# Kernel tuning notes

Measured on AMD Instinct MI355X. Metric: run time of the kernel, lower is better.

The kernel has to match this reference:

```python
import jax, jax.numpy as jnp
import numpy as np

# static config matching init_kwargs / input_specs
SPATIAL = [(64, 64), (32, 32), (16, 16), (8, 8)]  # (H_l, W_l) per level
LEN = sum(h * w for h, w in SPATIAL)  # 5440
B, C, H, L, P = 4, 256, 8, 4, 4
DH = C // H
DFF = 1024
EPS = 1e-5


def layer_norm(x, g, b):
    m = x.mean(-1, keepdims=True)
    v = ((x - m) ** 2).mean(-1, keepdims=True)
    return (x - m) / jnp.sqrt(v + EPS) * g + b


def msda_core(value, sampling_locations, attn_weights):
    """Multi-scale deformable attention core (bilinear sample + weighted sum).
    value: [B, Len, H, DH]; sampling_locations: [B, Lq, H, L, P, 2] in [0,1];
    attn_weights: [B, Lq, H, L, P]. Returns [B, Lq, C].
    Matches grid_sample(bilinear, align_corners=False, padding_mode='zeros')."""
    Bn, Lq = sampling_locations.shape[0], sampling_locations.shape[1]
    out = jnp.zeros((Bn, H, Lq, DH), value.dtype)
    start = 0
    for l, (Hl, Wl) in enumerate(SPATIAL):
        vl = value[:, start:start + Hl * Wl]          # [B, Hl*Wl, H, DH]
        start += Hl * Wl
        vl = vl.transpose(0, 2, 1, 3)                  # [B, H, Hl*Wl, DH]
        loc = sampling_locations[:, :, :, l].transpose(0, 2, 1, 3, 4)  # [B,H,Lq,P,2]
        # align_corners=False: pixel = loc * size - 0.5
        px = loc[..., 0] * Wl - 0.5
        py = loc[..., 1] * Hl - 0.5
        x0 = jnp.floor(px); y0 = jnp.floor(py)
        wx1 = px - x0; wy1 = py - y0
        x0i = x0.astype(jnp.int32); y0i = y0.astype(jnp.int32)
        samp = jnp.zeros((Bn, H, Lq, P, DH), value.dtype)
        for dx, dy in ((0, 0), (1, 0), (0, 1), (1, 1)):
            ix = x0i + dx; iy = y0i + dy
            w = (wx1 if dx else 1.0 - wx1) * (wy1 if dy else 1.0 - wy1)
            valid = (ix >= 0) & (ix < Wl) & (iy >= 0) & (iy < Hl)
            idx = jnp.clip(iy, 0, Hl - 1) * Wl + jnp.clip(ix, 0, Wl - 1)  # [B,H,Lq,P]
            g = jnp.take_along_axis(vl, idx.reshape(Bn, H, -1)[..., None], axis=2)
            g = g.reshape(Bn, H, Lq, P, DH)
            samp = samp + g * (w * valid)[..., None]
        aw = attn_weights[:, :, :, l].transpose(0, 2, 1, 3)  # [B,H,Lq,P]
        out = out + (samp * aw[..., None]).sum(3)
    return out.transpose(0, 2, 1, 3).reshape(Bn, Lq, C)


def setup_inputs() -> dict:
    key = jax.random.key(0)
    ks = jax.random.split(key, 20)
    inp = {
        'src': jax.random.normal(ks[0], (B, LEN, C), jnp.float32),
        'pos': jax.random.normal(ks[1], (B, LEN, C), jnp.float32),
        'reference_points': jax.random.uniform(ks[2], (B, LEN, L, 2), jnp.float32),
        'spatial_shapes': jnp.array(SPATIAL, dtype=jnp.int32),
        'level_start_index': jnp.array(np.cumsum([0] + [h * w for h, w in SPATIAL[:-1]]), dtype=jnp.int32),
        'valid_ratios': jnp.ones((B, L, 2), jnp.float32),
        # MSDeformAttn params
        'w_off': jax.random.normal(ks[3], (C, H * L * P * 2), jnp.float32) * 0.01,
        'b_off': jax.random.normal(ks[4], (H * L * P * 2,), jnp.float32) * 0.5,
        'w_attn': jax.random.normal(ks[5], (C, H * L * P), jnp.float32) * 0.05,
        'b_attn': jnp.zeros((H * L * P,), jnp.float32),
        'w_val': jax.random.normal(ks[6], (C, C), jnp.float32) * 0.05,
        'b_val': jnp.zeros((C,), jnp.float32),
        'w_out': jax.random.normal(ks[7], (C, C), jnp.float32) * 0.05,
        'b_out': jnp.zeros((C,), jnp.float32),
        # norm1 + FFN + norm2 params
        'g1': jnp.ones((C,), jnp.float32), 'be1': jnp.zeros((C,), jnp.float32),
        'w1': jax.random.normal(ks[8], (C, DFF), jnp.float32) * 0.05,
        'b1': jnp.zeros((DFF,), jnp.float32),
        'w2': jax.random.normal(ks[9], (DFF, C), jnp.float32) * 0.05,
        'b2': jnp.zeros((C,), jnp.float32),
        'g2': jnp.ones((C,), jnp.float32), 'be2': jnp.zeros((C,), jnp.float32),
    }
    return inp


def reference(src, pos, reference_points, spatial_shapes, level_start_index, valid_ratios,
              w_off, b_off, w_attn, b_attn, w_val, b_val, w_out, b_out,
              g1, be1, w1, b1, w2, b2, g2, be2):
    Bn, Lq, _ = src.shape
    q = src + pos  # with_pos_embed
    off = (q @ w_off + b_off).reshape(Bn, Lq, H, L, P, 2)
    aw = jax.nn.softmax((q @ w_attn + b_attn).reshape(Bn, Lq, H, L * P), axis=-1)
    aw = aw.reshape(Bn, Lq, H, L, P)
    # offset normalizer is (W_l, H_l) per level
    norm = jnp.array([[w, h] for h, w in SPATIAL], dtype=src.dtype)  # [L, 2]
    loc = reference_points[:, :, None, :, None, :] + off / norm[None, None, None, :, None, :]
    value = (src @ w_val + b_val).reshape(Bn, Lq, H, DH)  # padding_mask is None
    attn_out = msda_core(value, loc, aw) @ w_out + b_out
    x = layer_norm(src + attn_out, g1, be1)
    ffn = jax.nn.relu(x @ w1 + b1) @ w2 + b2
    return layer_norm(x + ffn, g2, be2)
```

## Files before the change

### kernel.cpp

```cpp
#include <hip/hip_runtime.h>
#include <hip/hip_fp16.h>
#include <math.h>

#define LEN   5440
#define NTOK  21760
#define CDIM  256
#define HEADS 8
#define DFF   1024
#define LEPS  1e-5f

typedef __attribute__((ext_vector_type(8))) _Float16 f16x8;
typedef __attribute__((ext_vector_type(4))) float f32x4;

__device__ __forceinline__ float4 f4_add(float4 a, float4 b) {
    return make_float4(a.x + b.x, a.y + b.y, a.z + b.z, a.w + b.w);
}

__global__ __launch_bounds__(256) void pack_k(const float* __restrict__ w_off,
                                              const float* __restrict__ w_attn,
                                              const float* __restrict__ w_val,
                                              const float* __restrict__ b_off,
                                              const float* __restrict__ b_attn,
                                              const float* __restrict__ b_val,
                                              const float* __restrict__ w_out,
                                              const float* __restrict__ w1,
                                              const float* __restrict__ w2,
                                              __half* __restrict__ WcatT,
                                              __half* __restrict__ woutT,
                                              __half* __restrict__ w1T,
                                              __half* __restrict__ w2T,
                                              float* __restrict__ bcat) {
    const int i = blockIdx.x * 256 + threadIdx.x;
    if (i < 163840) {
        const int c = i >> 8, k = i & 255;
        float v;
        if (c < 256)      v = w_off[k * 256 + c];
        else if (c < 384) v = w_attn[k * 128 + (c - 256)];
        else              v = w_val[k * 256 + (c - 384)];
        WcatT[i] = __float2half(v);
    } else if (i < 229376) {
        const int j = i - 163840, c = j >> 8, k = j & 255;
        woutT[j] = __float2half(w_out[k * 256 + c]);
    } else if (i < 491520) {
        const int j = i - 229376, c = j >> 8, k = j & 255;
        w1T[j] = __float2half(w1[k * 1024 + c]);
    } else if (i < 753664) {
        const int j = i - 491520, c = j >> 10, k = j & 1023;
        w2T[j] = __float2half(w2[k * 256 + c]);
    }
    if (i < 640) {
        bcat[i] = (i < 256) ? b_off[i] : (i < 384) ? b_attn[i - 256] : b_val[i - 384];
    }
}

__global__ __launch_bounds__(256) void cvt_k(const float* __restrict__ src,
                                             const float* __restrict__ pos,
                                             __half* __restrict__ qh,
                                             __half* __restrict__ srch) {
    const size_t i = (size_t)blockIdx.x * 256 + threadIdx.x;
    float4 s = *(const float4*)&src[i * 4];
    float4 p = *(const float4*)&pos[i * 4];
    union { __half2 h[2]; uint2 u; } Q, S;
    Q.h[0] = __floats2half2_rn(s.x + p.x, s.y + p.y);
    Q.h[1] = __floats2half2_rn(s.z + p.z, s.w + p.w);
    S.h[0] = __floats2half2_rn(s.x, s.y);
    S.h[1] = __floats2half2_rn(s.z, s.w);
    *(uint2*)&qh[i * 4]   = Q.u;
    *(uint2*)&srch[i * 4] = S.u;
}

template <bool RELU, bool OUTF, bool OUTH>
__global__ __launch_bounds__(256) void hgemm_k(const __half* __restrict__ Aq,
                                               const __half* __restrict__ Av,
                                               const __half* __restrict__ Bt,
                                               const float* __restrict__ bias,
                                               float* __restrict__ Cf,
                                               __half* __restrict__ Ch,
                                               int Nn, int K, int colSwitch) {
    __shared__ __half As[128][40];
    __shared__ __half Bs[128][40];
    const int bx = blockIdx.x, by = blockIdx.y;
    const int tid = threadIdx.x;
    const int lane = tid & 63;
    const int wave = tid >> 6;
    const int wr = (wave >> 1) * 64;
    const int wc = (wave & 1) * 64;

    const __half* __restrict__ Ah = (bx * 128 < colSwitch) ? Aq : Av;
    const __half* Abase = Ah + (size_t)(by * 128) * K;
    const __half* Bbase = Bt + (size_t)(bx * 128) * K;

    const int srow = tid >> 1;
    const int sk = (tid & 1) * 16;

    f32x4 acc[4][4];
#pragma unroll
    for (int m = 0; m < 4; ++m)
#pragma unroll
        for (int n = 0; n < 4; ++n) acc[m][n] = (f32x4){0.f, 0.f, 0.f, 0.f};

    const int fr = lane & 15;
    const int fk = (lane >> 4) * 8;

    for (int k0 = 0; k0 < K; k0 += 32) {
        const uint4 a0 = *(const uint4*)&Abase[(size_t)srow * K + k0 + sk];
        const uint4 a1 = *(const uint4*)&Abase[(size_t)srow * K + k0 + sk + 8];
        const uint4 b0 = *(const uint4*)&Bbase[(size_t)srow * K + k0 + sk];
        const uint4 b1 = *(const uint4*)&Bbase[(size_t)srow * K + k0 + sk + 8];
        __syncthreads();
        *(uint4*)&As[srow][sk]     = a0;
        *(uint4*)&As[srow][sk + 8] = a1;
        *(uint4*)&Bs[srow][sk]     = b0;
        *(uint4*)&Bs[srow][sk + 8] = b1;
        __syncthreads();
        f16x8 af[4], bf[4];
#pragma unroll
        for (int m = 0; m < 4; ++m) af[m] = *(const f16x8*)&As[wr + m * 16 + fr][fk];
#pragma unroll
        for (int n = 0; n < 4; ++n) bf[n] = *(const f16x8*)&Bs[wc + n * 16 + fr][fk];
#pragma unroll
        for (int m = 0; m < 4; ++m)
#pragma unroll
            for (int n = 0; n < 4; ++n)
                acc[m][n] = __builtin_amdgcn_mfma_f32_16x16x32_f16(af[m], bf[n], acc[m][n], 0, 0, 0);
    }

    const int rowb = by * 128 + wr + (lane >> 4) * 4;
    const int colb = bx * 128 + wc + fr;
    float bn[4];
#pragma unroll
    for (int n = 0; n < 4; ++n) bn[n] = bias[colb + n * 16];
#pragma unroll
    for (int m = 0; m < 4; ++m) {
#pragma unroll
        for (int r = 0; r < 4; ++r) {
            const size_t ro = (size_t)(rowb + m * 16 + r) * Nn + colb;
#pragma unroll
            for (int n = 0; n < 4; ++n) {
                float v = acc[m][n][r] + bn[n];
                if (RELU) v = fmaxf(v, 0.f);
                if (OUTF) Cf[ro + n * 16] = v;
                if (OUTH) Ch[ro + n * 16] = __float2half(v);
            }
        }
    }
}

__global__ __launch_bounds__(256) void msda_kernel(const float* __restrict__ C1,
                                                   const float* __restrict__ refp,
                                                   __half* __restrict__ out) {
    const int tid  = threadIdx.x;
    const int g    = tid & 7;
    const int pair = tid >> 3;
    const int h    = pair & 7;
    const int n    = blockIdx.x * 4 + (pair >> 3);
    const int b    = n / LEN;
    const size_t rowb = (size_t)n * 640;

    float lg[16];
    float mx = -1e30f;
#pragma unroll
    for (int s = 0; s < 16; ++s) {
        lg[s] = C1[rowb + 256 + h * 16 + s];
        mx = fmaxf(mx, lg[s]);
    }
    float sum = 0.f;
#pragma unroll
    for (int s = 0; s < 16; ++s) {
        lg[s] = expf(lg[s] - mx);
        sum += lg[s];
    }
    const float inv = 1.f / sum;

    const int Wi[4] = {64, 32, 16, 8};
    const int st[4] = {0, 4096, 5120, 5376};
    float4 acc = make_float4(0.f, 0.f, 0.f, 0.f);
    const int vbase_h = 384 + h * 32 + g * 4;

#pragma unroll
    for (int l = 0; l < 4; ++l) {
        const int   W  = Wi[l];
        const float Wf = (float)W;
        const float rx = refp[((size_t)n * 4 + l) * 2 + 0];
        const float ry = refp[((size_t)n * 4 + l) * 2 + 1];
#pragma unroll
        for (int p = 0; p < 4; ++p) {
            const float aw = lg[l * 4 + p] * inv;
            const float ox = C1[rowb + (size_t)(((h * 4 + l) * 4 + p) * 2 + 0)];
            const float oy = C1[rowb + (size_t)(((h * 4 + l) * 4 + p) * 2 + 1)];
            const float lx = rx + ox / Wf;
            const float ly = ry + oy / Wf;
            const float px = lx * Wf - 0.5f;
            const float py = ly * Wf - 0.5f;
            const float x0f = floorf(px), y0f = floorf(py);
            const float wx1 = px - x0f, wy1 = py - y0f;
            const int x0 = (int)x0f, y0 = (int)y0f;
#pragma unroll
            for (int c = 0; c < 4; ++c) {
                const int dx = c & 1, dy = c >> 1;
                const int ix = x0 + dx, iy = y0 + dy;
                const float wgt = (dx ? wx1 : 1.f - wx1) * (dy ? wy1 : 1.f - wy1);
                const bool valid = (ix >= 0) && (ix < W) && (iy >= 0) && (iy < W);
                const int ixc = min(max(ix, 0), W - 1);
                const int iyc = min(max(iy, 0), W - 1);
                const int pos = st[l] + iyc * W + ixc;
                const float4 v = *(const float4*)&C1[((size_t)(b * LEN + pos)) * 640 + vbase_h];
                const float wa = valid ? (aw * wgt) : 0.f;
                acc.x = fmaf(wa, v.x, acc.x);
                acc.y = fmaf(wa, v.y, acc.y);
                acc.z = fmaf(wa, v.z, acc.z);
                acc.w = fmaf(wa, v.w, acc.w);
            }
        }
    }
    union { __half2 h[2]; uint2 u; } O;
    O.h[0] = __floats2half2_rn(acc.x, acc.y);
    O.h[1] = __floats2half2_rn(acc.z, acc.w);
    *(uint2*)&out[(size_t)n * 256 + h * 32 + g * 4] = O.u;
}

template <bool WH>
__global__ __launch_bounds__(256) void ln_kernel(const float* __restrict__ Y,
                                                 const float* __restrict__ R,
                                                 const float* __restrict__ gm,
                                                 const float* __restrict__ bt,
                                                 float* __restrict__ O,
                                                 __half* __restrict__ OH) {
    const int wave = threadIdx.x >> 6, lane = threadIdx.x & 63;
    const int n = blockIdx.x * 4 + wave;
    const size_t base = (size_t)n * 256 + lane * 4;
    float4 y = *(const float4*)&Y[base];
    float4 r = *(const float4*)&R[base];
    float4 v = f4_add(y, r);
    float s = v.x + v.y + v.z + v.w;
#pragma unroll
    for (int m = 1; m < 64; m <<= 1) s += __shfl_xor(s, m, 64);
    const float mean = s * (1.f / 256.f);
    const float dx = v.x - mean, dy = v.y - mean, dz = v.z - mean, dw = v.w - mean;
    float ss = dx * dx + dy * dy + dz * dz + dw * dw;
#pragma unroll
    for (int m = 1; m < 64; m <<= 1) ss += __shfl_xor(ss, m, 64);
    const float rstd = rsqrtf(ss * (1.f / 256.f) + LEPS);
    const float4 g4 = *(const float4*)&gm[lane * 4];
    const float4 b4 = *(const float4*)&bt[lane * 4];
    float4 o;
    o.x = dx * rstd * g4.x + b4.x;
    o.y = dy * rstd * g4.y + b4.y;
    o.z = dz * rstd * g4.z + b4.z;
    o.w = dw * rstd * g4.w + b4.w;
    *(float4*)&O[base] = o;
    if (WH) {
        union { __half2 h[2]; uint2 u; } H;
        H.h[0] = __floats2half2_rn(o.x, o.y);
        H.h[1] = __floats2half2_rn(o.z, o.w);
        *(uint2*)&OH[base] = H.u;
    }
}

extern "C" void kernel_launch(void* const* d_in, const int* in_sizes, int n_in,
                              void* d_out, int out_size, void* d_ws, size_t ws_size,
                              hipStream_t stream) {
    const float* src   = (const float*)d_in[0];
    const float* pos   = (const float*)d_in[1];
    const float* refp  = (const float*)d_in[2];
    const float* w_off  = (const float*)d_in[6];
    const float* b_off  = (const float*)d_in[7];
    const float* w_attn = (const float*)d_in[8];
    const float* b_attn = (const float*)d_in[9];
    const float* w_val  = (const float*)d_in[10];
    const float* b_val  = (const float*)d_in[11];
    const float* w_out  = (const float*)d_in[12];
    const float* b_out  = (const float*)d_in[13];
    const float* g1     = (const float*)d_in[14];
    const float* be1    = (const float*)d_in[15];
    const float* w1     = (const float*)d_in[16];
    const float* b1     = (const float*)d_in[17];
    const float* w2     = (const float*)d_in[18];
    const float* b2     = (const float*)d_in[19];
    const float* g2     = (const float*)d_in[20];
    const float* be2    = (const float*)d_in[21];

    float* ws = (float*)d_ws;
    float*  C1    = ws + 0;
    __half* msdah = (__half*)(ws + 13926400);
    float*  xbuf  = ws + 16711680;
    __half* xh    = (__half*)(ws + 22282240);
    __half* hh    = (__half*)(ws + 25067520);
    __half* qh    = (__half*)(ws + 36208640);
    __half* srch  = (__half*)(ws + 38993920);
    __half* WcatT = (__half*)(ws + 41779200);
    __half* woutT = (__half*)(ws + 41861120);
    __half* w1T   = (__half*)(ws + 41893888);
    __half* w2T   = (__half*)(ws + 42024960);
    float*  bcat  = ws + 42156032;
    float*  ybuf  = C1;

    pack_k<<<2944, 256, 0, stream>>>(w_off, w_attn, w_val, b_off, b_attn, b_val,
                                     w_out, w1, w2, WcatT, woutT, w1T, w2T, bcat);
    cvt_k<<<NTOK / 4, 256, 0, stream>>>(src, pos, qh, srch);

    hgemm_k<false, true, false><<<dim3(5, 170), 256, 0, stream>>>(
        qh, srch, WcatT, bcat, C1, ((__half*)0), 640, 256, 384);

    msda_kernel<<<NTOK / 4, 256, 0, stream>>>(C1, refp, msdah);

    hgemm_k<false, true, false><<<dim3(2, 170), 256, 0, stream>>>(
        msdah, msdah, woutT, b_out, ybuf, (__half*)0, 256, 256, 0);

    ln_kernel<true><<<NTOK / 4, 256, 0, stream>>>(ybuf, src, g1, be1, xbuf, xh);

    hgemm_k<true, false, true><<<dim3(8, 170), 256, 0, stream>>>(
        xh, xh, w1T, b1, (float*)0, hh, DFF, 256, 0);

    hgemm_k<false, true, false><<<dim3(2, 170), 256, 0, stream>>>(
        hh, hh, w2T, b2, ybuf, (__half*)0, 256, DFF, 0);

    ln_kernel<false><<<NTOK / 4, 256, 0, stream>>>(ybuf, xbuf, g2, be2, (float*)d_out, (__half*)0);
}
```

Baseline: 323.7 us.

## Fuse fp32-to-half conversion into GEMM, store value in fp16, restructure MSDA gather

Drops the separate conversion kernel. The first GEMM now reads fp32 src (plus pos for the offset and attention columns) and converts to half while loading its tiles. That GEMM writes the offset and logit columns as fp32 with a 384 stride, and writes the value projection as a separate fp16 buffer. The MSDA kernel is reorganised: 16 threads per (token, head) each compute one sample's softmax weight and bilinear indices into shared memory, then each thread gathers half2 channels from the fp16 value buffer. This cuts memory traffic and launches, at the cost of lower value precision and more conversion work inside the GEMM load loop.

Result: faster. 301.2 us (-7.0%).

```diff
diff --git a/kernel.cpp b/kernel.cpp
--- a/kernel.cpp
+++ b/kernel.cpp
@@ -53,30 +53,14 @@
     }
 }
 
-__global__ __launch_bounds__(256) void cvt_k(const float* __restrict__ src,
-                                             const float* __restrict__ pos,
-                                             __half* __restrict__ qh,
-                                             __half* __restrict__ srch) {
-    const size_t i = (size_t)blockIdx.x * 256 + threadIdx.x;
-    float4 s = *(const float4*)&src[i * 4];
-    float4 p = *(const float4*)&pos[i * 4];
-    union { __half2 h[2]; uint2 u; } Q, S;
-    Q.h[0] = __floats2half2_rn(s.x + p.x, s.y + p.y);
-    Q.h[1] = __floats2half2_rn(s.z + p.z, s.w + p.w);
-    S.h[0] = __floats2half2_rn(s.x, s.y);
-    S.h[1] = __floats2half2_rn(s.z, s.w);
-    *(uint2*)&qh[i * 4]   = Q.u;
-    *(uint2*)&srch[i * 4] = S.u;
-}
-
-template <bool RELU, bool OUTF, bool OUTH>
-__global__ __launch_bounds__(256) void hgemm_k(const __half* __restrict__ Aq,
-                                               const __half* __restrict__ Av,
+template <bool AF32, int OMODE>
+__global__ __launch_bounds__(256) void hgemm_k(const void* __restrict__ Ap,
+                                               const float* __restrict__ A2f,
                                                const __half* __restrict__ Bt,
                                                const float* __restrict__ bias,
                                                float* __restrict__ Cf,
                                                __half* __restrict__ Ch,
-                                               int Nn, int K, int colSwitch) {
+                                               int NnF, int NnH, int K, int colSwitch) {
     __shared__ __half As[128][40];
     __shared__ __half Bs[128][40];
     const int bx = blockIdx.x, by = blockIdx.y;
@@ -85,9 +69,8 @@
     const int wave = tid >> 6;
     const int wr = (wave >> 1) * 64;
     const int wc = (wave & 1) * 64;
-
-    const __half* __restrict__ Ah = (bx * 128 < colSwitch) ? Aq : Av;
-    const __half* Abase = Ah + (size_t)(by * 128) * K;
+    const bool useA2 = AF32 && (bx * 128 < colSwitch);
+
     const __half* Bbase = Bt + (size_t)(bx * 128) * K;
 
     const int srow = tid >> 1;
@@ -103,8 +86,36 @@
     const int fk = (lane >> 4) * 8;
 
     for (int k0 = 0; k0 < K; k0 += 32) {
-        const uint4 a0 = *(const uint4*)&Abase[(size_t)srow * K + k0 + sk];
-        const uint4 a1 = *(const uint4*)&Abase[(size_t)srow * K + k0 + sk + 8];
+        uint4 a0, a1;
+        if (AF32) {
+            const float* Af = (const float*)Ap + (size_t)(by * 128 + srow) * K + k0 + sk;
+            float4 f0 = *(const float4*)(Af + 0);
+            float4 f1 = *(const float4*)(Af + 4);
+            float4 f2 = *(const float4*)(Af + 8);
+            float4 f3 = *(const float4*)(Af + 12);
+            if (useA2) {
+                const float* Pf = A2f + (size_t)(by * 128 + srow) * K + k0 + sk;
+                f0 = f4_add(f0, *(const float4*)(Pf + 0));
+                f1 = f4_add(f1, *(const float4*)(Pf + 4));
+                f2 = f4_add(f2, *(const float4*)(Pf + 8));
+                f3 = f4_add(f3, *(const float4*)(Pf + 12));
+            }
+            union { __half2 h[8]; uint4 u[2]; } cv;
+            cv.h[0] = __floats2half2_rn(f0.x, f0.y);
+            cv.h[1] = __floats2half2_rn(f0.z, f0.w);
+            cv.h[2] = __floats2half2_rn(f1.x, f1.y);
+            cv.h[3] = __floats2half2_rn(f1.z, f1.w);
+            cv.h[4] = __floats2half2_rn(f2.x, f2.y);
+            cv.h[5] = __floats2half2_rn(f2.z, f2.w);
+            cv.h[6] = __floats2half2_rn(f3.x, f3.y);
+            cv.h[7] = __floats2half2_rn(f3.z, f3.w);
+            a0 = cv.u[0];
+            a1 = cv.u[1];
+        } else {
+            const __half* Ah = (const __half*)Ap + (size_t)(by * 128 + srow) * K + k0 + sk;
+            a0 = *(const uint4*)(Ah + 0);
+            a1 = *(const uint4*)(Ah + 8);
+        }
         const uint4 b0 = *(const uint4*)&Bbase[(size_t)srow * K + k0 + sk];
         const uint4 b1 = *(const uint4*)&Bbase[(size_t)srow * K + k0 + sk + 8];
         __syncthreads();
@@ -130,93 +141,105 @@
     float bn[4];
 #pragma unroll
     for (int n = 0; n < 4; ++n) bn[n] = bias[colb + n * 16];
+    const bool vhalf = (OMODE == 2) || (OMODE == 3 && bx * 128 >= colSwitch);
+    const int colh = (OMODE == 3) ? (colb - colSwitch) : colb;
 #pragma unroll
     for (int m = 0; m < 4; ++m) {
 #pragma unroll
         for (int r = 0; r < 4; ++r) {
-            const size_t ro = (size_t)(rowb + m * 16 + r) * Nn + colb;
+            const int row = rowb + m * 16 + r;
 #pragma unroll
             for (int n = 0; n < 4; ++n) {
                 float v = acc[m][n][r] + bn[n];
-                if (RELU) v = fmaxf(v, 0.f);
-                if (OUTF) Cf[ro + n * 16] = v;
-                if (OUTH) Ch[ro + n * 16] = __float2half(v);
+                if (OMODE == 2) v = fmaxf(v, 0.f);
+                if (vhalf) Ch[(size_t)row * NnH + colh + n * 16] = __float2half(v);
+                else       Cf[(size_t)row * NnF + colb + n * 16] = v;
             }
         }
     }
 }
 
-__global__ __launch_bounds__(256) void msda_kernel(const float* __restrict__ C1,
+__global__ __launch_bounds__(256) void msda_kernel(const float* __restrict__ C1a,
+                                                   const __half* __restrict__ Vh,
                                                    const float* __restrict__ refp,
                                                    __half* __restrict__ out) {
-    const int tid  = threadIdx.x;
-    const int g    = tid & 7;
-    const int pair = tid >> 3;
-    const int h    = pair & 7;
-    const int n    = blockIdx.x * 4 + (pair >> 3);
-    const int b    = n / LEN;
-    const size_t rowb = (size_t)n * 640;
-
-    float lg[16];
-    float mx = -1e30f;
-#pragma unroll
-    for (int s = 0; s < 16; ++s) {
-        lg[s] = C1[rowb + 256 + h * 16 + s];
-        mx = fmaxf(mx, lg[s]);
-    }
-    float sum = 0.f;
-#pragma unroll
-    for (int s = 0; s < 16; ++s) {
-        lg[s] = expf(lg[s] - mx);
-        sum += lg[s];
-    }
-    const float inv = 1.f / sum;
-
-    const int Wi[4] = {64, 32, 16, 8};
-    const int st[4] = {0, 4096, 5120, 5376};
-    float4 acc = make_float4(0.f, 0.f, 0.f, 0.f);
-    const int vbase_h = 384 + h * 32 + g * 4;
-
-#pragma unroll
-    for (int l = 0; l < 4; ++l) {
-        const int   W  = Wi[l];
+    __shared__ int   sIdx[16][17][4];
+    __shared__ float sW[16][17][4];
+    const int tid = threadIdx.x;
+    const int gi = tid >> 4;
+    const int si = tid & 15;
+    const int n = blockIdx.x * 2 + (gi >> 3);
+    const int h = gi & 7;
+    const int b = n / LEN;
+
+    {
+        const int l = si >> 2, p = si & 3;
+        const float lg = C1a[(size_t)n * 384 + 256 + h * 16 + si];
+        float mx = lg;
+#pragma unroll
+        for (int m = 1; m < 16; m <<= 1) mx = fmaxf(mx, __shfl_xor(mx, m, 16));
+        const float e = expf(lg - mx);
+        float sum = e;
+#pragma unroll
+        for (int m = 1; m < 16; m <<= 1) sum += __shfl_xor(sum, m, 16);
+        const float aw = e / sum;
+
+        const int Wi[4] = {64, 32, 16, 8};
+        const int st[4] = {0, 4096, 5120, 5376};
+        const int W = Wi[l];
         const float Wf = (float)W;
         const float rx = refp[((size_t)n * 4 + l) * 2 + 0];
         const float ry = refp[((size_t)n * 4 + l) * 2 + 1];
-#pragma unroll
-        for (int p = 0; p < 4; ++p) {
-            const float aw = lg[l * 4 + p] * inv;
-            const float ox = C1[rowb + (size_t)(((h * 4 + l) * 4 + p) * 2 + 0)];
-            const float oy = C1[rowb + (size_t)(((h * 4 + l) * 4 + p) * 2 + 1)];
-            const float lx = rx + ox / Wf;
-            const float ly = ry + oy / Wf;
-            const float px = lx * Wf - 0.5f;
-            const float py = ly * Wf - 0.5f;
-            const float x0f = floorf(px), y0f = floorf(py);
-            const float wx1 = px - x0f, wy1 = py - y0f;
-            const int x0 = (int)x0f, y0 = (int)y0f;
-#pragma unroll
-            for (int c = 0; c < 4; ++c) {
-                const int dx = c & 1, dy = c >> 1;
-                const int ix = x0 + dx, iy = y0 + dy;
-                const float wgt = (dx ? wx1 : 1.f - wx1) * (dy ? wy1 : 1.f - wy1);
-                const bool valid = (ix >= 0) && (ix < W) && (iy >= 0) && (iy < W);
-                const int ixc = min(max(ix, 0), W - 1);
-                const int iyc = min(max(iy, 0), W - 1);
-                const int pos = st[l] + iyc * W + ixc;
-                const float4 v = *(const float4*)&C1[((size_t)(b * LEN + pos)) * 640 + vbase_h];
-                const float wa = valid ? (aw * wgt) : 0.f;
-                acc.x = fmaf(wa, v.x, acc.x);
-                acc.y = fmaf(wa, v.y, acc.y);
-                acc.z = fmaf(wa, v.z, acc.z);
-                acc.w = fmaf(wa, v.w, acc.w);
-            }
-        }
-    }
-    union { __half2 h[2]; uint2 u; } O;
-    O.h[0] = __floats2half2_rn(acc.x, acc.y);
-    O.h[1] = __floats2half2_rn(acc.z, acc.w);
-    *(uint2*)&out[(size_t)n * 256 + h * 32 + g * 4] = O.u;
+        const float ox = C1a[(size_t)n * 384 + (((h * 4 + l) * 4 + p) * 2 + 0)];
+        const float oy = C1a[(size_t)n * 384 + (((h * 4 + l) * 4 + p) * 2 + 1)];
+        const float lx = rx + ox / Wf;
+        const float ly = ry + oy / Wf;
+        const float px = lx * Wf - 0.5f;
+        const float py = ly * Wf - 0.5f;
+        const float x0f = floorf(px), y0f = floorf(py);
+        const float wx1 = px - x0f, wy1 = py - y0f;
+        const int x0 = (int)x0f, y0 = (int)y0f;
+#pragma unroll
+        for (int c = 0; c < 4; ++c) {
+            const int dx = c & 1, dy = c >> 1;
+            const int ix = x0 + dx, iy = y0 + dy;
+            const float wgt = (dx ? wx1 : 1.f - wx1) * (dy ? wy1 : 1.f - wy1);
+            const bool valid = (ix >= 0) && (ix < W) && (iy >= 0) && (iy < W);
+            const int ixc = min(max(ix, 0), W - 1);
+            const int iyc = min(max(iy, 0), W - 1);
+            const int pos = st[l] + iyc * W + ixc;
+            sIdx[gi][si][c] = ((b * LEN + pos) << 8) + h * 32;
+            sW[gi][si][c] = valid ? (aw * wgt) : 0.f;
+        }
+    }
+    __syncthreads();
+
+    float accx = 0.f, accy = 0.f;
+    const int ch = si * 2;
+#pragma unroll
+    for (int s = 0; s < 16; ++s) {
+        const int4   idx = *(const int4*)&sIdx[gi][s][0];
+        const float4 w   = *(const float4*)&sW[gi][s][0];
+        {
+            const float2 v = __half22float2(*(const __half2*)&Vh[idx.x + ch]);
+            accx = fmaf(w.x, v.x, accx); accy = fmaf(w.x, v.y, accy);
+        }
+        {
+            const float2 v = __half22float2(*(const __half2*)&Vh[idx.y + ch]);
+            accx = fmaf(w.y, v.x, accx); accy = fmaf(w.y, v.y, accy);
+        }
+        {
+            const float2 v = __half22float2(*(const __half2*)&Vh[idx.z + ch]);
+            accx = fmaf(w.z, v.x, accx); accy = fmaf(w.z, v.y, accy);
+        }
+        {
+            const float2 v = __half22float2(*(const __half2*)&Vh[idx.w + ch]);
+            accx = fmaf(w.w, v.x, accx); accy = fmaf(w.w, v.y, accy);
+        }
+    }
+    union { __half2 h2; unsigned u; } O;
+    O.h2 = __floats2half2_rn(accx, accy);
+    *(unsigned*)&out[(size_t)n * 256 + h * 32 + ch] = O.u;
 }
 
 template <bool WH>
@@ -250,10 +273,10 @@
     o.w = dw * rstd * g4.w + b4.w;
     *(float4*)&O[base] = o;
     if (WH) {
-        union { __half2 h[2]; uint2 u; } H;
-        H.h[0] = __floats2half2_rn(o.x, o.y);
-        H.h[1] = __floats2half2_rn(o.z, o.w);
-        *(uint2*)&OH[base] = H.u;
+        union { __half2 h[2]; uint2 u; } Hh;
+        Hh.h[0] = __floats2half2_rn(o.x, o.y);
+        Hh.h[1] = __floats2half2_rn(o.z, o.w);
+        *(uint2*)&OH[base] = Hh.u;
     }
 }
 
@@ -281,39 +304,37 @@
     const float* be2    = (const float*)d_in[21];
 
     float* ws = (float*)d_ws;
-    float*  C1    = ws + 0;
-    __half* msdah = (__half*)(ws + 13926400);
-    float*  xbuf  = ws + 16711680;
-    __half* xh    = (__half*)(ws + 22282240);
-    __half* hh    = (__half*)(ws + 25067520);
-    __half* qh    = (__half*)(ws + 36208640);
-    __half* srch  = (__half*)(ws + 38993920);
-    __half* WcatT = (__half*)(ws + 41779200);
-    __half* woutT = (__half*)(ws + 41861120);
-    __half* w1T   = (__half*)(ws + 41893888);
-    __half* w2T   = (__half*)(ws + 42024960);
-    float*  bcat  = ws + 42156032;
-    float*  ybuf  = C1;
+    float*  C1a   = ws + 0;
+    __half* Vh    = (__half*)(ws + 8355840);
+    __half* msdah = (__half*)(ws + 11141120);
+    float*  xbuf  = ws + 13926400;
+    __half* xh    = (__half*)(ws + 19496960);
+    __half* hh    = (__half*)(ws + 22282240);
+    __half* WcatT = (__half*)(ws + 33423360);
+    __half* woutT = (__half*)(ws + 33505280);
+    __half* w1T   = (__half*)(ws + 33538048);
+    __half* w2T   = (__half*)(ws + 33669120);
+    float*  bcat  = ws + 33800192;
+    float*  ybuf  = C1a;
 
     pack_k<<<2944, 256, 0, stream>>>(w_off, w_attn, w_val, b_off, b_attn, b_val,
                                      w_out, w1, w2, WcatT, woutT, w1T, w2T, bcat);
-    cvt_k<<<NTOK / 4, 256, 0, stream>>>(src, pos, qh, srch);
-
-    hgemm_k<false, true, false><<<dim3(5, 170), 256, 0, stream>>>(
-        qh, srch, WcatT, bcat, C1, ((__half*)0), 640, 256, 384);
-
-    msda_kernel<<<NTOK / 4, 256, 0, stream>>>(C1, refp, msdah);
-
-    hgemm_k<false, true, false><<<dim3(2, 170), 256, 0, stream>>>(
-        msdah, msdah, woutT, b_out, ybuf, (__half*)0, 256, 256, 0);
+
+    hgemm_k<true, 3><<<dim3(5, 170), 256, 0, stream>>>(
+        (const void*)src, pos, WcatT, bcat, C1a, Vh, 384, 256, 256, 384);
+
+    msda_kernel<<<NTOK / 2, 256, 0, stream>>>(C1a, Vh, refp, msdah);
+
+    hgemm_k<false, 0><<<dim3(2, 170), 256, 0, stream>>>(
+        (const void*)msdah, nullptr, woutT, b_out, ybuf, nullptr, 256, 256, 256, 0);
 
     ln_kernel<true><<<NTOK / 4, 256, 0, stream>>>(ybuf, src, g1, be1, xbuf, xh);
 
-    hgemm_k<true, false, true><<<dim3(8, 170), 256, 0, stream>>>(
-        xh, xh, w1T, b1, (float*)0, hh, DFF, 256, 0);
-
-    hgemm_k<false, true, false><<<dim3(2, 170), 256, 0, stream>>>(
-        hh, hh, w2T, b2, ybuf, (__half*)0, 256, DFF, 0);
-
-    ln_kernel<false><<<NTOK / 4, 256, 0, stream>>>(ybuf, xbuf, g2, be2, (float*)d_out, (__half*)0);
-}
+    hgemm_k<false, 2><<<dim3(8, 170), 256, 0, stream>>>(
+        (const void*)xh, nullptr, w1T, b1, nullptr, hh, 1024, 1024, 256, 0);
+
+    hgemm_k<false, 0><<<dim3(2, 170), 256, 0, stream>>>(
+        (const void*)hh, nullptr, w2T, b2, ybuf, nullptr, 256, 256, 1024, 0);
+
+    ln_kernel<false><<<NTOK / 4, 256, 0, stream>>>(ybuf, xbuf, g2, be2, (float*)d_out, nullptr);
+}
```
